# Optimization experiments

Hardware: AMD Instinct MI355X
Metric: run time of the kernel (lower is better)

The kernel has to match this reference:

```python
import jax, jax.numpy as jnp
import numpy as np

BATCH, IN_F, OUT_F = 1024, 512, 512
GRID_SIZE, SPLINE_ORDER = 32, 3
P_DEACTIVATE = 0.1


def b_splines(x, grid, k):
    """x: (n, in), grid: (in, G+2k+1) -> bases (n, in, G+k). Cox-de Boor recursion."""
    x = x[..., None]  # (n, in, 1)
    bases = ((x >= grid[:, :-1]) & (x < grid[:, 1:])).astype(x.dtype)
    for j in range(1, k + 1):
        left = (x - grid[:, : -(j + 1)]) / (grid[:, j:-1] - grid[:, : -(j + 1)])
        right = (grid[:, j + 1:] - x) / (grid[:, j + 1:] - grid[:, 1:-j])
        bases = left * bases[..., :-1] + right * bases[..., 1:]
    return bases


def setup_inputs() -> dict:
    key = jax.random.key(0)
    k1, k2, k3, k4, k5 = jax.random.split(key, 5)
    # uniform extended grid over [-1, 1], same for every input feature
    h = 2.0 / GRID_SIZE
    knots = np.arange(-SPLINE_ORDER, GRID_SIZE + SPLINE_ORDER + 1, dtype=np.float32) * h - 1.0
    grid = jnp.asarray(np.tile(knots, (IN_F, 1)))  # (in, G+2k+1)
    return {
        "x": jax.random.normal(k1, (BATCH, IN_F), jnp.float32),
        "base_weight": jax.random.normal(k2, (OUT_F, IN_F), jnp.float32) * 0.05,
        "spline_weight": jax.random.normal(k3, (OUT_F, IN_F, GRID_SIZE + SPLINE_ORDER), jnp.float32) * 0.1,
        "spline_scaler": jax.random.normal(k4, (OUT_F, IN_F), jnp.float32),
        "grid": grid,
        "deactivate_mask": jax.random.bernoulli(k5, P_DEACTIVATE, (OUT_F, IN_F)),
    }


def reference(x, base_weight, spline_weight, spline_scaler, grid, deactivate_mask):
    k = SPLINE_ORDER
    weights = spline_weight * spline_scaler[..., None]  # scaled_spline_weight (o, i, c)
    # base path: F.linear(silu(x), base_weight)
    base_out = jax.nn.silu(x) @ base_weight.T  # (b, o)
    # spline path
    bases = b_splines(x, grid, k)  # (b, i, c)
    contrib = jnp.einsum('bic,oic->boi', bases, weights)  # (b, o, i)
    # linear fallback from spline values at grid endpoints
    gmin = grid[:, k].min()
    gmax = grid[:, -k - 1].max()
    ends_x = jnp.stack([gmin, gmax])[:, None] * jnp.ones((1, x.shape[1]), x.dtype)  # (2, i)
    y_ends = jnp.einsum('nic,oic->noi', b_splines(ends_x, grid, k), weights)  # (2, o, i)
    y_start, y_end = y_ends[0], y_ends[1]
    dx = gmax - gmin
    degenerate = jnp.abs(dx) < 1e-8
    a = jnp.where(degenerate, 0.0, (y_end - y_start) / jnp.where(degenerate, 1.0, dx))  # (o, i)
    b = y_start - a * gmin
    lin = a[None] * x[:, None, :] + b[None]  # (b, o, i)
    final = jnp.where(deactivate_mask[None], lin, contrib)
    return base_out + final.sum(axis=2)
```

## Files before the change

### kernel.cpp

```cpp
#include <hip/hip_runtime.h>
#include <hip/hip_bf16.h>


typedef unsigned short u16;
typedef unsigned int u32;
typedef unsigned long long u64;
typedef __attribute__((ext_vector_type(8))) short short8;
typedef __attribute__((ext_vector_type(4))) float floatx4;

#define IN_F 512
#define OUT_F 512
#define BATCH 1024
#define K_SPLINE (IN_F * 36)
#define K_BASE_OFF K_SPLINE
#define K_LIN_OFF (K_SPLINE + IN_F)
#define K_TOT (K_SPLINE + 2 * IN_F)
#define SPLITS 16
#define KPS 1216
#define NIT 19
#define MN (BATCH * OUT_F)

static __device__ inline u16 f2b(float f) {
  union { float f; u32 u; } v; v.f = f;
  u32 r = v.u + 0x7FFFu + ((v.u >> 16) & 1u);
  return (u16)(r >> 16);
}
static __device__ inline float b2f(u32 lo16) {
  union { u32 u; float f; } v; v.u = lo16 << 16; return v.f;
}

__global__ __launch_bounds__(256) void prep_kernel(
    const float* __restrict__ bw, const float* __restrict__ sw,
    const float* __restrict__ sc, const void* __restrict__ maskp,
    const float* __restrict__ x, u16* __restrict__ B,
    float* __restrict__ bias_part, u16* __restrict__ A) {
  __shared__ __align__(16) u64 lds64[1120 * 4];
  __shared__ int sflag;
  __shared__ float ws4[4];
  int blk = blockIdx.x, t = threadIdx.x;

  if (blk >= 1024) {
    int bix = blk - 1024;
    int b = bix >> 1;
    int i0 = (bix & 1) << 8;
    int i = i0 + t;
    float xv = x[(size_t)b * IN_F + i];

    u64* myrow = lds64 + t * 9;
#pragma unroll
    for (int j = 0; j < 9; ++j) myrow[j] = 0;

    int mc = (int)floorf((xv + 1.1875f) * 16.0f);
    float gm = (float)mc * 0.0625f - 1.1875f;
    if (xv < gm) { mc -= 1; gm -= 0.0625f; }
    else if (xv >= gm + 0.0625f) { mc += 1; gm += 0.0625f; }
    if (mc >= 0 && mc <= 37) {
      float t_ = (xv - gm) * 16.0f;
      float t2 = t_ * t_, t3 = t2 * t_;
      float omt = 1.0f - t_;
      u16 r0 = f2b(omt * omt * omt * (1.0f / 6.0f));
      u16 r1 = f2b((3.0f * t3 - 6.0f * t2 + 4.0f) * (1.0f / 6.0f));
      u16 r2 = f2b((-3.0f * t3 + 3.0f * t2 + 3.0f * t_ + 1.0f) * (1.0f / 6.0f));
      float f0 = b2f(r0), f1 = b2f(r1), f2 = b2f(r2);
      u16 bv[4] = {r0, r1, r2, f2b(1.0f - f0 - f1 - f2)};
      u16* lds_u = (u16*)lds64;
#pragma unroll
      for (int j = 0; j < 4; ++j) {
        int c = mc - 3 + j;
        if ((u32)c < 35u) lds_u[t * 36 + c] = bv[j];
      }
    }
    __syncthreads();

    u64* dstA = (u64*)(A + (size_t)b * K_TOT + (size_t)i0 * 36);
#pragma unroll
    for (int j = 0; j < 9; ++j) dstA[j * 256 + t] = lds64[j * 256 + t];

    float sl = xv / (1.0f + __expf(-xv));
    A[(size_t)b * K_TOT + K_BASE_OFF + i] = f2b(sl);
    A[(size_t)b * K_TOT + K_LIN_OFF + i] = f2b(xv);
    return;
  }

  float* lds_f = (float*)lds64;
  int id = blk * 256 + t;
  int o = id >> 9, i = id & 511;
  int i0 = (blk & 1) * 256;

  const float* swb = sw + ((size_t)o * 512 + i0) * 35;
  const floatx4* sw4 = (const floatx4*)swb;
  floatx4* lds4 = (floatx4*)lds_f;
#pragma unroll
  for (int j = 0; j < 8; ++j) lds4[j * 256 + t] = sw4[j * 256 + t];
  if (t < 192) lds4[8 * 256 + t] = sw4[8 * 256 + t];

  const u32* mw = (const u32*)maskp;
  if (t == 0) sflag = 0;
  __syncthreads();
  if (t < 64) {
    u32 w2 = mw[blk * 64 + t];
    if ((w2 & 0xFFFFFF00u) && w2 != 0x3F800000u) atomicOr(&sflag, 1);
  }
  __syncthreads();
  int fl = sflag;
  if (!(fl & 1)) {
    u32 w1 = mw[blk * 256 + t];
    if (w1 == 0x3F800000u) atomicOr(&sflag, 2);
  }
  __syncthreads();
  fl = sflag;
  bool mk;
  if (fl & 1)      mk = ((const unsigned char*)maskp)[id] != 0;
  else if (fl & 2) mk = ((const float*)maskp)[id] != 0.0f;
  else             mk = ((const int*)maskp)[id] != 0;

  float s = sc[id];
  float w[35];
#pragma unroll
  for (int c = 0; c < 35; ++c) w[c] = lds_f[t * 35 + c] * s;
  __syncthreads();

  float ys = (w[0] + 4.0f * w[1] + w[2]) * (1.0f / 6.0f);
  float ye = (w[32] + 4.0f * w[33] + w[34]) * (1.0f / 6.0f);
  float a = (ye - ys) * 0.5f;
  float bl = ys + a;

  union { u16 r16[36]; u64 r64[9]; } ur;
#pragma unroll
  for (int c = 0; c < 35; ++c) ur.r16[c] = f2b(mk ? 0.0f : w[c]);
  ur.r16[35] = 0;
  u64* myrow = lds64 + t * 9;
#pragma unroll
  for (int j = 0; j < 9; ++j) myrow[j] = ur.r64[j];

  B[(size_t)o * K_TOT + K_BASE_OFF + i] = f2b(bw[id]);
  B[(size_t)o * K_TOT + K_LIN_OFF + i] = f2b(mk ? a : 0.0f);

  float v = mk ? bl : 0.0f;
#pragma unroll
  for (int off = 32; off >= 1; off >>= 1) v += __shfl_down(v, off);
  if ((t & 63) == 0) ws4[t >> 6] = v;
  __syncthreads();
  if (t == 0) bias_part[blk] = ws4[0] + ws4[1] + ws4[2] + ws4[3];

  u64* dst = (u64*)(B + (size_t)o * K_TOT + (size_t)i0 * 36);
#pragma unroll
  for (int j = 0; j < 9; ++j) dst[j * 256 + t] = lds64[j * 256 + t];
}

__global__ __launch_bounds__(512, 2) void gemm_fused(const u16* __restrict__ A,
                                                     const u16* __restrict__ Bp,
                                                     u16* __restrict__ P) {
  __shared__ u16 As[2][256 * 64];
  __shared__ u16 Bs[2][128 * 64];

  int t = threadIdx.x;
  int p = blockIdx.x;
  int tile = p & 15, ks = p >> 4;
  int bm = tile >> 2, bn = tile & 3;

  int w = t >> 6, l = t & 63;
  int wm = w & 3, wn = w >> 2;

  floatx4 acc[4][4];
#pragma unroll
  for (int pp = 0; pp < 4; ++pp)
#pragma unroll
    for (int q = 0; q < 4; ++q) acc[pp][q] = (floatx4)0.0f;

  int k0s = ks * KPS;

  int ra = t >> 3;
  int cg = (t & 7) ^ (ra & 7);
  const u16* Agp = A + (size_t)(bm * 256 + ra) * K_TOT + k0s + cg * 8;
  const u16* Bgp = Bp + (size_t)(bn * 128 + ra) * K_TOT + k0s + cg * 8;

  int mr = l & 15;
  int cq = l >> 4;

#define STAGE(buf, koff)                                                       \
  do {                                                                         \
    const u16* a_ = Agp + (koff);                                              \
    const u16* b_ = Bgp + (koff);                                              \
    __builtin_amdgcn_global_load_lds(                                          \
        (const __attribute__((address_space(1))) void*)a_,                     \
        (__attribute__((address_space(3))) void*)(&As[buf][t * 8]), 16, 0, 0); \
    __builtin_amdgcn_global_load_lds(                                          \
        (const __attribute__((address_space(1))) void*)(a_ + (size_t)64 * K_TOT),   \
        (__attribute__((address_space(3))) void*)(&As[buf][4096 + t * 8]), 16, 0, 0);\
    __builtin_amdgcn_global_load_lds(                                          \
        (const __attribute__((address_space(1))) void*)(a_ + (size_t)128 * K_TOT),  \
        (__attribute__((address_space(3))) void*)(&As[buf][8192 + t * 8]), 16, 0, 0);\
    __builtin_amdgcn_global_load_lds(                                          \
        (const __attribute__((address_space(1))) void*)(a_ + (size_t)192 * K_TOT),  \
        (__attribute__((address_space(3))) void*)(&As[buf][12288 + t * 8]), 16, 0, 0);\
    __builtin_amdgcn_global_load_lds(                                          \
        (const __attribute__((address_space(1))) void*)b_,                     \
        (__attribute__((address_space(3))) void*)(&Bs[buf][t * 8]), 16, 0, 0); \
    __builtin_amdgcn_global_load_lds(                                          \
        (const __attribute__((address_space(1))) void*)(b_ + (size_t)64 * K_TOT),   \
        (__attribute__((address_space(3))) void*)(&Bs[buf][4096 + t * 8]), 16, 0, 0);\
  } while (0)

  STAGE(0, 0);

  for (int kk = 0; kk < NIT; ++kk) {
    int cur = kk & 1;
    if (kk + 1 < NIT) {
      STAGE(cur ^ 1, (kk + 1) * 64);
      asm volatile("s_waitcnt vmcnt(6)" ::: "memory");
    } else {
      asm volatile("s_waitcnt vmcnt(0)" ::: "memory");
    }
    __builtin_amdgcn_s_barrier();
    __builtin_amdgcn_sched_barrier(0);

    const u16* Ac = &As[cur][0];
    const u16* Bc = &Bs[cur][0];
#pragma unroll
    for (int h = 0; h < 2; ++h) {
      short8 af[4], bf[4];
      int c = h * 4 + cq;
#pragma unroll
      for (int tm = 0; tm < 4; ++tm) {
        int row = wm * 64 + tm * 16 + mr;
        af[tm] = *(const short8*)&Ac[row * 64 + ((c ^ (row & 7)) << 3)];
      }
#pragma unroll
      for (int tn = 0; tn < 4; ++tn) {
        int row = wn * 64 + tn * 16 + mr;
        bf[tn] = *(const short8*)&Bc[row * 64 + ((c ^ (row & 7)) << 3)];
      }
#pragma unroll
      for (int tm = 0; tm < 4; ++tm)
#pragma unroll
        for (int tn = 0; tn < 4; ++tn)
          acc[tm][tn] = __builtin_amdgcn_mfma_f32_16x16x32_bf16(af[tm], bf[tn], acc[tm][tn], 0, 0, 0);
    }

    __builtin_amdgcn_s_barrier();
    __builtin_amdgcn_sched_barrier(0);
  }
#undef STAGE

  u16* Pb = P + ((size_t)tile * SPLITS + ks) * 32768;
#pragma unroll
  for (int q = 0; q < 8; ++q) {
    int tm = q >> 1, tn0 = (q & 1) * 2;
    u16 r[8];
#pragma unroll
    for (int z = 0; z < 4; ++z) r[z] = f2b(acc[tm][tn0][z]);
#pragma unroll
    for (int z = 0; z < 4; ++z) r[4 + z] = f2b(acc[tm][tn0 + 1][z]);
    *(short8*)(Pb + q * 4096 + t * 8) = *(short8*)r;
  }
}

__global__ __launch_bounds__(256) void reduce_kernel(const u16* __restrict__ P,
                                                     const float* __restrict__ bias_part,
                                                     float* __restrict__ out) {
  int rid = blockIdx.x * 256 + threadIdx.x;
  int tile = rid >> 12;
  int rem = rid & 4095;
  int q = rem >> 9, t = rem & 511;
  const u16* base = P + (size_t)tile * SPLITS * 32768 + q * 4096 + t * 8;

  float s[8] = {0, 0, 0, 0, 0, 0, 0, 0};
#pragma unroll
  for (int ks = 0; ks < SPLITS; ++ks) {
    short8 v = *(const short8*)(base + (size_t)ks * 32768);
#pragma unroll
    for (int j = 0; j < 8; ++j) s[j] += b2f((u32)(u16)v[j]);
  }

  int w = t >> 6, l = t & 63;
  int wm = w & 3, wn = w >> 2;
  int bm = tile >> 2, bn = tile & 3;
  int row0 = bm * 256 + wm * 64 + ((l >> 4) << 2);
  int col0 = bn * 128 + wn * 64 + (l & 15);
  int tm = q >> 1, tn0 = (q & 1) * 2;
#pragma unroll
  for (int j = 0; j < 8; ++j) {
    int tn = tn0 + (j >> 2), rr = j & 3;
    int row = row0 + tm * 16 + rr;
    int col = col0 + tn * 16;
    float bsv = bias_part[2 * col] + bias_part[2 * col + 1];
    out[(size_t)row * OUT_F + col] = s[j] + bsv;
  }
}

extern "C" void kernel_launch(void* const* d_in, const int* in_sizes, int n_in,
                              void* d_out, int out_size, void* d_ws, size_t ws_size,
                              hipStream_t stream) {
  const float* x  = (const float*)d_in[0];
  const float* bw = (const float*)d_in[1];
  const float* sw = (const float*)d_in[2];
  const float* sc = (const float*)d_in[3];
  const void* mask = d_in[5];

  const size_t B_BYTES = (size_t)OUT_F * K_TOT * 2;
  const size_t BIAS_OFF = B_BYTES;
  const size_t A_OFF = B_BYTES + 8192;
  const size_t A_BYTES = (size_t)BATCH * K_TOT * 2;
  const size_t P_OFF = A_OFF + A_BYTES;

  char* wsb = (char*)d_ws;
  u16* Bpack = (u16*)wsb;
  float* bias_part = (float*)(wsb + BIAS_OFF);
  u16* Adense = (u16*)(wsb + A_OFF);
  u16* P = (u16*)(wsb + P_OFF);

  prep_kernel<<<3072, 256, 0, stream>>>(bw, sw, sc, mask, x, Bpack, bias_part, Adense);
  gemm_fused<<<256, 512, 0, stream>>>(Adense, Bpack, P);
  reduce_kernel<<<256, 256, 0, stream>>>(P, bias_part, (float*)d_out);
}
```

Baseline: 134.5 us.

## Replace double-buffered 64-wide K tiles with 4-slot ring of 32-wide stages

The GEMM main loop moves from two 64-wide K buffers to a four-slot ring of 32-wide K stages, keeping three stages in flight. LDS fragment reads for the current stage are issued before the next prefetch and barrier, and the MFMA block is wrapped in s_setprio to favour math issue. The aim is deeper prefetch to hide global-load latency. The cost is twice as many loop iterations and barriers, plus a narrower 4-way XOR swizzle that may raise LDS bank conflicts.

```diff
diff --git a/kernel.cpp b/kernel.cpp
--- a/kernel.cpp
+++ b/kernel.cpp
@@ -17,7 +17,7 @@
 #define K_TOT (K_SPLINE + 2 * IN_F)
 #define SPLITS 16
 #define KPS 1216
-#define NIT 19
+#define NHALF 38
 #define MN (BATCH * OUT_F)
 
 static __device__ inline u16 f2b(float f) {
@@ -151,8 +151,7 @@
 __global__ __launch_bounds__(512, 2) void gemm_fused(const u16* __restrict__ A,
                                                      const u16* __restrict__ Bp,
                                                      u16* __restrict__ P) {
-  __shared__ u16 As[2][256 * 64];
-  __shared__ u16 Bs[2][128 * 64];
+  __shared__ u16 ring[4][12288];
 
   int t = threadIdx.x;
   int p = blockIdx.x;
@@ -170,78 +169,77 @@
 
   int k0s = ks * KPS;
 
-  int ra = t >> 3;
-  int cg = (t & 7) ^ (ra & 7);
-  const u16* Agp = A + (size_t)(bm * 256 + ra) * K_TOT + k0s + cg * 8;
-  const u16* Bgp = Bp + (size_t)(bn * 128 + ra) * K_TOT + k0s + cg * 8;
+  int ra2 = t >> 2;
+  int cg2 = (t & 3) ^ (ra2 & 3);
+  const u16* Ag2 = A + (size_t)(bm * 256 + ra2) * K_TOT + k0s + cg2 * 8;
+  const u16* Bg2 = Bp + (size_t)(bn * 128 + ra2) * K_TOT + k0s + cg2 * 8;
 
   int mr = l & 15;
   int cq = l >> 4;
 
-#define STAGE(buf, koff)                                                       \
+#define STAGEH(slot, koff)                                                     \
   do {                                                                         \
-    const u16* a_ = Agp + (koff);                                              \
-    const u16* b_ = Bgp + (koff);                                              \
+    const u16* a_ = Ag2 + (koff);                                              \
+    const u16* b_ = Bg2 + (koff);                                              \
+    u16* s_ = &ring[slot][0];                                                  \
     __builtin_amdgcn_global_load_lds(                                          \
         (const __attribute__((address_space(1))) void*)a_,                     \
-        (__attribute__((address_space(3))) void*)(&As[buf][t * 8]), 16, 0, 0); \
-    __builtin_amdgcn_global_load_lds(                                          \
-        (const __attribute__((address_space(1))) void*)(a_ + (size_t)64 * K_TOT),   \
-        (__attribute__((address_space(3))) void*)(&As[buf][4096 + t * 8]), 16, 0, 0);\
+        (__attribute__((address_space(3))) void*)(s_ + t * 8), 16, 0, 0);      \
     __builtin_amdgcn_global_load_lds(                                          \
         (const __attribute__((address_space(1))) void*)(a_ + (size_t)128 * K_TOT),  \
-        (__attribute__((address_space(3))) void*)(&As[buf][8192 + t * 8]), 16, 0, 0);\
-    __builtin_amdgcn_global_load_lds(                                          \
-        (const __attribute__((address_space(1))) void*)(a_ + (size_t)192 * K_TOT),  \
-        (__attribute__((address_space(3))) void*)(&As[buf][12288 + t * 8]), 16, 0, 0);\
+        (__attribute__((address_space(3))) void*)(s_ + 4096 + t * 8), 16, 0, 0);    \
     __builtin_amdgcn_global_load_lds(                                          \
         (const __attribute__((address_space(1))) void*)b_,                     \
-        (__attribute__((address_space(3))) void*)(&Bs[buf][t * 8]), 16, 0, 0); \
-    __builtin_amdgcn_global_load_lds(                                          \
-        (const __attribute__((address_space(1))) void*)(b_ + (size_t)64 * K_TOT),   \
-        (__attribute__((address_space(3))) void*)(&Bs[buf][4096 + t * 8]), 16, 0, 0);\
+        (__attribute__((address_space(3))) void*)(s_ + 8192 + t * 8), 16, 0, 0);    \
   } while (0)
 
-  STAGE(0, 0);
-
-  for (int kk = 0; kk < NIT; ++kk) {
-    int cur = kk & 1;
-    if (kk + 1 < NIT) {
-      STAGE(cur ^ 1, (kk + 1) * 64);
+  STAGEH(0, 0);
+  STAGEH(1, 32);
+  STAGEH(2, 64);
+  asm volatile("s_waitcnt vmcnt(6)" ::: "memory");
+  __builtin_amdgcn_s_barrier();
+  __builtin_amdgcn_sched_barrier(0);
+
+  for (int m = 0; m < NHALF; ++m) {
+    int slot = m & 3;
+    const u16* Acs = &ring[slot][0];
+    const u16* Bcs = &ring[slot][8192];
+
+    short8 af[4], bf[4];
+#pragma unroll
+    for (int tm = 0; tm < 4; ++tm) {
+      int row = wm * 64 + tm * 16 + mr;
+      af[tm] = *(const short8*)&Acs[row * 32 + ((cq ^ (row & 3)) << 3)];
+    }
+#pragma unroll
+    for (int tn = 0; tn < 4; ++tn) {
+      int row = wn * 64 + tn * 16 + mr;
+      bf[tn] = *(const short8*)&Bcs[row * 32 + ((cq ^ (row & 3)) << 3)];
+    }
+
+    if (m < NHALF - 3) {
+      STAGEH((m + 3) & 3, (m + 3) * 32);
       asm volatile("s_waitcnt vmcnt(6)" ::: "memory");
-    } else {
+    } else if (m == NHALF - 3) {
+      asm volatile("s_waitcnt vmcnt(3)" ::: "memory");
+    } else if (m == NHALF - 2) {
       asm volatile("s_waitcnt vmcnt(0)" ::: "memory");
     }
     __builtin_amdgcn_s_barrier();
     __builtin_amdgcn_sched_barrier(0);
 
-    const u16* Ac = &As[cur][0];
-    const u16* Bc = &Bs[cur][0];
-#pragma unroll
-    for (int h = 0; h < 2; ++h) {
-      short8 af[4], bf[4];
-      int c = h * 4 + cq;
-#pragma unroll
-      for (int tm = 0; tm < 4; ++tm) {
-        int row = wm * 64 + tm * 16 + mr;
-        af[tm] = *(const short8*)&Ac[row * 64 + ((c ^ (row & 7)) << 3)];
-      }
-#pragma unroll
-      for (int tn = 0; tn < 4; ++tn) {
-        int row = wn * 64 + tn * 16 + mr;
-        bf[tn] = *(const short8*)&Bc[row * 64 + ((c ^ (row & 7)) << 3)];
-      }
-#pragma unroll
-      for (int tm = 0; tm < 4; ++tm)
-#pragma unroll
-        for (int tn = 0; tn < 4; ++tn)
-          acc[tm][tn] = __builtin_amdgcn_mfma_f32_16x16x32_bf16(af[tm], bf[tn], acc[tm][tn], 0, 0, 0);
-    }
+    __builtin_amdgcn_s_setprio(1);
+#pragma unroll
+    for (int tm = 0; tm < 4; ++tm)
+#pragma unroll
+      for (int tn = 0; tn < 4; ++tn)
+        acc[tm][tn] = __builtin_amdgcn_mfma_f32_16x16x32_bf16(af[tm], bf[tn], acc[tm][tn], 0, 0, 0);
+    __builtin_amdgcn_s_setprio(0);
 
     __builtin_amdgcn_s_barrier();
     __builtin_amdgcn_sched_barrier(0);
   }
-#undef STAGE
+#undef STAGEH
 
   u16* Pb = P + ((size_t)tile * SPLITS + ks) * 32768;
 #pragma unroll
```

Measured after the change: 134.9 us. No clear change (+0.3%).
